# Performance work log

Measured on AMD Instinct MI355X. Metric: run time of the kernel, lower is better.

## Reference

```python
import jax, jax.numpy as jnp
import numpy as np

N_FEAT = 11   # players+ball features
HID = 48      # GAT hidden dim
HEADS = 4
GRU = 64
B = 64        # chains
T = 16        # frames per chain
NPG = 23      # nodes per frame graph (22 players + ball)
G = B * T
NTOT = G * NPG
FRAME = 2 * HID  # mean||max pool


def setup_inputs() -> dict:
    key = jax.random.key(0)
    ks = jax.random.split(key, 24)
    # block-diagonal fully-connected (with self loops) edge_index per graph
    base = np.arange(NPG)
    src = np.repeat(base, NPG)
    dst = np.tile(base, NPG)
    off = (np.arange(G) * NPG)[:, None]
    edge_index = np.stack([(src[None] + off).ravel(), (dst[None] + off).ravel()]).astype(np.int64)
    batch = np.repeat(np.arange(G), NPG).astype(np.int64)

    def p(k, shape, scale=0.1):
        return jax.random.normal(k, shape, jnp.float32) * scale

    return dict(
        x=jax.random.normal(ks[0], (NTOT, N_FEAT), jnp.float32),
        edge_index=jnp.asarray(edge_index), batch=jnp.asarray(batch),
        W1=p(ks[1], (N_FEAT, HEADS * HID)), as1=p(ks[2], (HEADS, HID)), ad1=p(ks[3], (HEADS, HID)), b1=p(ks[4], (HEADS * HID,)),
        W2=p(ks[5], (HEADS * HID, HID)), as2=p(ks[6], (1, HID)), ad2=p(ks[7], (1, HID)), b2=p(ks[8], (HID,)),
        Wih0=p(ks[9], (3 * GRU, FRAME)), Whh0=p(ks[10], (3 * GRU, GRU)), bih0=p(ks[11], (3 * GRU,)), bhh0=p(ks[12], (3 * GRU,)),
        Wih1=p(ks[13], (3 * GRU, GRU)), Whh1=p(ks[14], (3 * GRU, GRU)), bih1=p(ks[15], (3 * GRU,)), bhh1=p(ks[16], (3 * GRU,)),
        Wh1=p(ks[17], (GRU, 32)), bh1=p(ks[18], (32,)), Wh2=p(ks[19], (32, 1)), bh2=p(ks[20], (1,)),
    )


def _gat(x, src, dst, W, a_s, a_d, b, heads, concat):
    # PyG GATConv: per-head linear, edge score LeakyReLU(a_s.h_i + a_d.h_j),
    # softmax over incoming edges (by dst), weighted aggregation of h_src.
    h = (x @ W).reshape(-1, heads, HID)            # [N,H,D]
    al_s = (h * a_s).sum(-1)                       # [N,H]
    al_d = (h * a_d).sum(-1)
    e = jax.nn.leaky_relu(al_s[src] + al_d[dst], 0.2)  # [E,H]
    m = jax.ops.segment_max(e, dst, num_segments=NTOT)
    w = jnp.exp(e - m[dst])
    s = jax.ops.segment_sum(w, dst, num_segments=NTOT)
    alpha = w / (s[dst] + 1e-16)
    out = jax.ops.segment_sum(h[src] * alpha[:, :, None], dst, num_segments=NTOT)  # [N,H,D]
    if concat:
        return out.reshape(NTOT, heads * HID) + b
    return out.mean(1) + b


def _gru_layer(xs, Wih, Whh, bih, bhh):
    # torch.nn.GRU single layer, batch_first; xs: [B,T,in]
    def step(h, x_t):
        gi = x_t @ Wih.T + bih
        gh = h @ Whh.T + bhh
        ir, iz, in_ = jnp.split(gi, 3, -1)
        hr, hz, hn = jnp.split(gh, 3, -1)
        r = jax.nn.sigmoid(ir + hr)
        z = jax.nn.sigmoid(iz + hz)
        n = jnp.tanh(in_ + r * hn)
        h2 = (1 - z) * n + z * h
        return h2, h2
    h0 = jnp.zeros((xs.shape[0], GRU), xs.dtype)
    _, out = jax.lax.scan(step, h0, jnp.swapaxes(xs, 0, 1))
    return jnp.swapaxes(out, 0, 1)


def reference(x, edge_index, batch, W1, as1, ad1, b1, W2, as2, ad2, b2,
              Wih0, Whh0, bih0, bhh0, Wih1, Whh1, bih1, bhh1, Wh1, bh1, Wh2, bh2):
    src, dst = edge_index[0], edge_index[1]
    h = jax.nn.elu(_gat(x, src, dst, W1, as1, ad1, b1, HEADS, True))   # [N,192]
    h = jax.nn.elu(_gat(h, src, dst, W2, as2, ad2, b2, 1, False))      # [N,48]
    mean = jax.ops.segment_sum(h, batch, num_segments=G) / NPG
    mx = jax.ops.segment_max(h, batch, num_segments=G)
    frames = jnp.concatenate([mean, mx], -1).reshape(B, T, FRAME)      # [B,T,96]
    h1 = _gru_layer(frames, Wih0, Whh0, bih0, bhh0)
    h2 = _gru_layer(h1, Wih1, Whh1, bih1, bhh1)
    last = h2[:, -1]                                                   # [B,64]
    logits = jax.nn.relu(last @ Wh1 + bh1) @ Wh2 + bh2                 # [B,1]
    return logits[:, 0]
```

## Files before the change

### kernel.cpp

```cpp
#include <hip/hip_runtime.h>
#include <math.h>

#define NPG    23
#define HID    48
#define HEADS  4
#define C1     192
#define NFEAT  11
#define GG     1024
#define GRUH   64
#define FRAME  96
#define TT     16
#define BB     64

#define HSTR   196
#define GSTR   52

#define OFF_X    0
#define OFF_ALS  256
#define OFF_ALD  348
#define OFF_H    440
#define OFF_H1   4948
#define LDSF     9456

__device__ __forceinline__ float elu_(float v) {
    return (v > 0.f) ? v : (__expf(v) - 1.f);
}

#define PHASE_FENCE() __builtin_amdgcn_sched_barrier(0)

__global__ __launch_bounds__(256, 2) void gat_fused(
    const float* __restrict__ x,
    const float* __restrict__ W1,
    const float* __restrict__ as1,
    const float* __restrict__ ad1,
    const float* __restrict__ b1,
    const float* __restrict__ W2,
    const float* __restrict__ as2,
    const float* __restrict__ ad2,
    const float* __restrict__ b2,
    float* __restrict__ frames)
{
    __shared__ float S[LDSF];
    float* s_x    = S + OFF_X;
    float* s_als  = S + OFF_ALS;
    float* s_ald  = S + OFF_ALD;
    float* s_h    = S + OFF_H;
    float* s_h1   = S + OFF_H1;
    float* s_g    = S + OFF_H;
    float* s_h2   = S + OFF_H + NPG * GSTR;
    float* s_als2 = S + OFF_X;
    float* s_ald2 = S + OFF_X + NPG;

    const int g   = blockIdx.x;
    const int tid = threadIdx.x;

    for (int i = tid; i < NPG * NFEAT; i += 256) s_x[i] = x[g * NPG * NFEAT + i];
    if (tid < 184) s_als[tid] = 0.f;
    __syncthreads();
    PHASE_FENCE();

    if (tid < 240) {
        const int c4 = tid % 48, ng = tid / 48;
        const int hh = c4 / 12;
        float4 acc[5];
        #pragma unroll
        for (int nn = 0; nn < 5; nn++) acc[nn] = make_float4(0.f, 0.f, 0.f, 0.f);
        #pragma unroll 1
        for (int k = 0; k < NFEAT; k++) {
            const float4 w = *(const float4*)(W1 + k * C1 + 4 * c4);
            #pragma unroll
            for (int nn = 0; nn < 5; nn++) {
                int n = ng * 5 + nn; n = (n < NPG) ? n : NPG - 1;
                const float xv = s_x[n * NFEAT + k];
                acc[nn].x += xv * w.x; acc[nn].y += xv * w.y;
                acc[nn].z += xv * w.z; acc[nn].w += xv * w.w;
            }
        }
        const float4 a_s = *(const float4*)(as1 + 4 * c4);
        const float4 a_d = *(const float4*)(ad1 + 4 * c4);
        #pragma unroll
        for (int nn = 0; nn < 5; nn++) {
            const int n = ng * 5 + nn;
            if (n < NPG) {
                *(float4*)(s_h + n * HSTR + 4 * c4) = acc[nn];
                atomicAdd(&s_als[hh * NPG + n],
                          acc[nn].x * a_s.x + acc[nn].y * a_s.y + acc[nn].z * a_s.z + acc[nn].w * a_s.w);
                atomicAdd(&s_ald[hh * NPG + n],
                          acc[nn].x * a_d.x + acc[nn].y * a_d.y + acc[nn].z * a_d.z + acc[nn].w * a_d.w);
            }
        }
    }
    __syncthreads();
    PHASE_FENCE();

    if (tid < 184) {
        const int j = tid >> 3, sub = tid & 7;
        const int hh = sub >> 1, half = sub & 1;
        const float ald_j = s_ald[hh * NPG + j];
        float a[NPG];
        float m = -1e30f;
        #pragma unroll
        for (int i = 0; i < NPG; i++) {
            float e = s_als[hh * NPG + i] + ald_j;
            e = (e > 0.f) ? e : 0.2f * e;
            a[i] = e;
            m = fmaxf(m, e);
        }
        float ssum = 0.f;
        #pragma unroll
        for (int i = 0; i < NPG; i++) {
            const float w = __expf(a[i] - m);
            a[i] = w;
            ssum += w;
        }
        const float inv = 1.f / (ssum + 1e-16f);
        const int cb = hh * HID + half * 24;
        #pragma unroll 1
        for (int c4 = 0; c4 < 6; c4++) {
            float4 acc = make_float4(0.f, 0.f, 0.f, 0.f);
            #pragma unroll
            for (int i = 0; i < NPG; i++) {
                const float4 hv = *(const float4*)(s_h + i * HSTR + cb + 4 * c4);
                acc.x += a[i] * hv.x; acc.y += a[i] * hv.y;
                acc.z += a[i] * hv.z; acc.w += a[i] * hv.w;
            }
            const float4 bb = *(const float4*)(b1 + cb + 4 * c4);
            float4 v;
            v.x = elu_(acc.x * inv + bb.x);
            v.y = elu_(acc.y * inv + bb.y);
            v.z = elu_(acc.z * inv + bb.z);
            v.w = elu_(acc.w * inv + bb.w);
            *(float4*)(s_h1 + j * HSTR + cb + 4 * c4) = v;
        }
    } else if (tid < 184 + 46) {
        s_als2[tid - 184] = 0.f;
    }
    __syncthreads();
    PHASE_FENCE();

    if (tid < 192) {
        const int kc  = tid & 3;
        const int rem = tid >> 2;
        const int c4  = rem % 12, ng = rem / 12;
        float4 acc[6];
        #pragma unroll
        for (int nn = 0; nn < 6; nn++) acc[nn] = make_float4(0.f, 0.f, 0.f, 0.f);
        #pragma unroll 1
        for (int k4 = 0; k4 < 12; k4++) {
            const int kk = kc * 12 + k4;
            const float* w2p = W2 + (4 * kk) * HID + 4 * c4;
            const float4 r0 = *(const float4*)(w2p);
            const float4 r1 = *(const float4*)(w2p + HID);
            const float4 r2 = *(const float4*)(w2p + 2 * HID);
            const float4 r3 = *(const float4*)(w2p + 3 * HID);
            #pragma unroll
            for (int nn = 0; nn < 6; nn++) {
                int n = ng * 6 + nn; n = (n < NPG) ? n : NPG - 1;
                const float4 hv = *(const float4*)(s_h1 + n * HSTR + 4 * kk);
                acc[nn].x += hv.x*r0.x + hv.y*r1.x + hv.z*r2.x + hv.w*r3.x;
                acc[nn].y += hv.x*r0.y + hv.y*r1.y + hv.z*r2.y + hv.w*r3.y;
                acc[nn].z += hv.x*r0.z + hv.y*r1.z + hv.z*r2.z + hv.w*r3.z;
                acc[nn].w += hv.x*r0.w + hv.y*r1.w + hv.z*r2.w + hv.w*r3.w;
            }
        }
        #pragma unroll
        for (int nn = 0; nn < 6; nn++) {
            float4 a = acc[nn];
            a.x += __shfl_xor(a.x, 1); a.x += __shfl_xor(a.x, 2);
            a.y += __shfl_xor(a.y, 1); a.y += __shfl_xor(a.y, 2);
            a.z += __shfl_xor(a.z, 1); a.z += __shfl_xor(a.z, 2);
            a.w += __shfl_xor(a.w, 1); a.w += __shfl_xor(a.w, 2);
            acc[nn] = a;
        }
        if (kc == 0) {
            const float4 a_s = *(const float4*)(as2 + 4 * c4);
            const float4 a_d = *(const float4*)(ad2 + 4 * c4);
            #pragma unroll
            for (int nn = 0; nn < 6; nn++) {
                const int n = ng * 6 + nn;
                if (n < NPG) {
                    *(float4*)(s_g + n * GSTR + 4 * c4) = acc[nn];
                    atomicAdd(&s_als2[n],
                              acc[nn].x*a_s.x + acc[nn].y*a_s.y + acc[nn].z*a_s.z + acc[nn].w*a_s.w);
                    atomicAdd(&s_ald2[n],
                              acc[nn].x*a_d.x + acc[nn].y*a_d.y + acc[nn].z*a_d.z + acc[nn].w*a_d.w);
                }
            }
        }
    }
    __syncthreads();
    PHASE_FENCE();

    if (tid < 48) {
        const int q = tid & 3, jp = tid >> 2;
        const int j0 = 2 * jp, j1 = 2 * jp + 1;
        const bool has1 = (j1 < NPG);
        const int cb = q * 12;
        const float ald0 = s_ald2[j0];
        const float ald1 = has1 ? s_ald2[j1] : 0.f;
        float m0 = -1e30f, m1 = -1e30f;
        #pragma unroll
        for (int i = 0; i < NPG; i++) {
            const float ai = s_als2[i];
            float e0 = ai + ald0; e0 = (e0 > 0.f) ? e0 : 0.2f * e0;
            float e1 = ai + ald1; e1 = (e1 > 0.f) ? e1 : 0.2f * e1;
            m0 = fmaxf(m0, e0); m1 = fmaxf(m1, e1);
        }
        float4 acc0[3], acc1[3];
        #pragma unroll
        for (int c = 0; c < 3; c++) {
            acc0[c] = make_float4(0.f, 0.f, 0.f, 0.f);
            acc1[c] = make_float4(0.f, 0.f, 0.f, 0.f);
        }
        float ss0 = 0.f, ss1 = 0.f;
        #pragma unroll 1
        for (int i = 0; i < NPG; i++) {
            const float ai = s_als2[i];
            float e0 = ai + ald0; e0 = (e0 > 0.f) ? e0 : 0.2f * e0;
            float e1 = ai + ald1; e1 = (e1 > 0.f) ? e1 : 0.2f * e1;
            const float p0 = __expf(e0 - m0); ss0 += p0;
            const float p1 = __expf(e1 - m1); ss1 += p1;
            const float* gp = s_g + i * GSTR + cb;
            #pragma unroll
            for (int c = 0; c < 3; c++) {
                const float4 gv = *(const float4*)(gp + 4 * c);
                acc0[c].x += p0 * gv.x; acc0[c].y += p0 * gv.y;
                acc0[c].z += p0 * gv.z; acc0[c].w += p0 * gv.w;
                acc1[c].x += p1 * gv.x; acc1[c].y += p1 * gv.y;
                acc1[c].z += p1 * gv.z; acc1[c].w += p1 * gv.w;
            }
        }
        const float inv0 = 1.f / (ss0 + 1e-16f);
        const float inv1 = 1.f / (ss1 + 1e-16f);
        #pragma unroll
        for (int c = 0; c < 3; c++) {
            const float4 bb = *(const float4*)(b2 + cb + 4 * c);
            float4 v;
            v.x = elu_(acc0[c].x * inv0 + bb.x);
            v.y = elu_(acc0[c].y * inv0 + bb.y);
            v.z = elu_(acc0[c].z * inv0 + bb.z);
            v.w = elu_(acc0[c].w * inv0 + bb.w);
            *(float4*)(s_h2 + j0 * HID + cb + 4 * c) = v;
            if (has1) {
                v.x = elu_(acc1[c].x * inv1 + bb.x);
                v.y = elu_(acc1[c].y * inv1 + bb.y);
                v.z = elu_(acc1[c].z * inv1 + bb.z);
                v.w = elu_(acc1[c].w * inv1 + bb.w);
                *(float4*)(s_h2 + j1 * HID + cb + 4 * c) = v;
            }
        }
    }
    __syncthreads();
    PHASE_FENCE();

    if (tid < HID) {
        float sm = 0.f, mx = -1e30f;
        #pragma unroll
        for (int j = 0; j < NPG; j++) {
            const float v = s_h2[j * HID + tid];
            sm += v; mx = fmaxf(mx, v);
        }
        frames[g * FRAME + tid]       = sm * (1.0f / NPG);
        frames[g * FRAME + HID + tid] = mx;
    }
}

__global__ __launch_bounds__(384) void gru_head(
    const float* __restrict__ frames,
    const float* __restrict__ Wih0,
    const float* __restrict__ bih0,
    const float* __restrict__ Whh0,
    const float* __restrict__ bhh0,
    const float* __restrict__ Wih1,
    const float* __restrict__ bih1,
    const float* __restrict__ Whh1,
    const float* __restrict__ bhh1,
    const float* __restrict__ Wh1,
    const float* __restrict__ bh1,
    const float* __restrict__ Wh2,
    const float* __restrict__ bh2,
    float* __restrict__ out)
{
    __shared__ float s_f[TT * FRAME];
    __shared__ float s_gi0[TT * C1];
    __shared__ float s_h0[GRUH], s_h1[GRUH];
    __shared__ float s_gh0[C1], s_gi1[C1], s_gh1[C1];
    __shared__ float s_t1[32];

    const int b = blockIdx.x, tid = threadIdx.x;

    {
        const float4* src = (const float4*)(frames + b * TT * FRAME);
        ((float4*)s_f)[tid] = src[tid];
    }
    if (tid < GRUH) { s_h0[tid] = 0.f; s_h1[tid] = 0.f; }
    __syncthreads();

    {
        const int c = tid % C1, tp = tid / C1;
        float accg[8];
        const float b0 = bih0[c];
        #pragma unroll
        for (int tt = 0; tt < 8; tt++) accg[tt] = b0;
        const float4* wr = (const float4*)(Wih0 + c * FRAME);
        const float4* f4 = (const float4*)s_f;
        #pragma unroll 4
        for (int k4 = 0; k4 < FRAME / 4; k4++) {
            const float4 w = wr[k4];
            #pragma unroll
            for (int tt = 0; tt < 8; tt++) {
                const float4 f = f4[(tt * 2 + tp) * (FRAME / 4) + k4];
                accg[tt] += w.x * f.x + w.y * f.y + w.z * f.z + w.w * f.w;
            }
        }
        #pragma unroll
        for (int tt = 0; tt < 8; tt++) s_gi0[(tt * 2 + tp) * C1 + c] = accg[tt];
    }

    const int row = tid >> 1, kh = tid & 1;
    float w0[32], w1[32], w2[32];
    {
        const float4* p0 = (const float4*)(Whh0 + row * 64 + kh * 32);
        const float4* p1 = (const float4*)(Wih1 + row * 64 + kh * 32);
        const float4* p2 = (const float4*)(Whh1 + row * 64 + kh * 32);
        #pragma unroll
        for (int k4 = 0; k4 < 8; k4++) {
            const float4 v0 = p0[k4];
            w0[4*k4] = v0.x; w0[4*k4+1] = v0.y; w0[4*k4+2] = v0.z; w0[4*k4+3] = v0.w;
            const float4 v1 = p1[k4];
            w1[4*k4] = v1.x; w1[4*k4+1] = v1.y; w1[4*k4+2] = v1.z; w1[4*k4+3] = v1.w;
            const float4 v2 = p2[k4];
            w2[4*k4] = v2.x; w2[4*k4+1] = v2.y; w2[4*k4+2] = v2.z; w2[4*k4+3] = v2.w;
        }
    }
    const float bh0r = kh ? 0.f : bhh0[row];
    const float bi1r = kh ? 0.f : bih1[row];
    const float bh1r = kh ? 0.f : bhh1[row];
    __syncthreads();

    for (int it = 0; it <= TT; it++) {
        {
            float s0 = bh0r, s1 = bi1r, s2 = bh1r;
            const float4* h0v = (const float4*)(s_h0 + kh * 32);
            const float4* h1v = (const float4*)(s_h1 + kh * 32);
            #pragma unroll
            for (int k4 = 0; k4 < 8; k4++) {
                const float4 a = h0v[k4];
                const float4 c = h1v[k4];
                s0 += w0[4*k4]*a.x + w0[4*k4+1]*a.y + w0[4*k4+2]*a.z + w0[4*k4+3]*a.w;
                s1 += w1[4*k4]*a.x + w1[4*k4+1]*a.y + w1[4*k4+2]*a.z + w1[4*k4+3]*a.w;
                s2 += w2[4*k4]*c.x + w2[4*k4+1]*c.y + w2[4*k4+2]*c.z + w2[4*k4+3]*c.w;
            }
            s0 += __shfl_xor(s0, 1, 64);
            s1 += __shfl_xor(s1, 1, 64);
            s2 += __shfl_xor(s2, 1, 64);
            if (kh == 0) { s_gh0[row] = s0; s_gi1[row] = s1; s_gh1[row] = s2; }
        }
        __syncthreads();
        if (tid < GRUH) {
            if (it < TT) {
                const float ir = s_gi0[it*C1 + tid];
                const float iz = s_gi0[it*C1 + 64 + tid];
                const float in_ = s_gi0[it*C1 + 128 + tid];
                const float hr = s_gh0[tid], hz = s_gh0[64 + tid], hn = s_gh0[128 + tid];
                const float r = 1.f / (1.f + __expf(-(ir + hr)));
                const float z = 1.f / (1.f + __expf(-(iz + hz)));
                const float nx = in_ + r * hn;
                const float e2 = __expf(2.f * nx);
                const float n = (e2 - 1.f) / (e2 + 1.f);
                s_h0[tid] = (1.f - z) * n + z * s_h0[tid];
            }
        } else if (tid < 2 * GRUH) {
            if (it >= 1) {
                const int c = tid - GRUH;
                const float ir = s_gi1[c], iz = s_gi1[64 + c], in_ = s_gi1[128 + c];
                const float hr = s_gh1[c], hz = s_gh1[64 + c], hn = s_gh1[128 + c];
                const float r = 1.f / (1.f + __expf(-(ir + hr)));
                const float z = 1.f / (1.f + __expf(-(iz + hz)));
                const float nx = in_ + r * hn;
                const float e2 = __expf(2.f * nx);
                const float n = (e2 - 1.f) / (e2 + 1.f);
                s_h1[c] = (1.f - z) * n + z * s_h1[c];
            }
        }
        __syncthreads();
    }

    if (tid < 32) {
        float s = bh1[tid];
        #pragma unroll
        for (int k = 0; k < GRUH; k++) s += s_h1[k] * Wh1[k * 32 + tid];
        s_t1[tid] = fmaxf(s, 0.f);
    }
    __syncthreads();
    if (tid == 0) {
        float s = bh2[0];
        #pragma unroll
        for (int k = 0; k < 32; k++) s += s_t1[k] * Wh2[k];
        out[b] = s;
    }
}

extern "C" void kernel_launch(void* const* d_in, const int* in_sizes, int n_in,
                              void* d_out, int out_size, void* d_ws, size_t ws_size,
                              hipStream_t stream) {
    const float* x    = (const float*)d_in[0];
    const float* W1   = (const float*)d_in[3];
    const float* as1  = (const float*)d_in[4];
    const float* ad1  = (const float*)d_in[5];
    const float* b1   = (const float*)d_in[6];
    const float* W2   = (const float*)d_in[7];
    const float* as2  = (const float*)d_in[8];
    const float* ad2  = (const float*)d_in[9];
    const float* b2   = (const float*)d_in[10];
    const float* Wih0 = (const float*)d_in[11];
    const float* Whh0 = (const float*)d_in[12];
    const float* bih0 = (const float*)d_in[13];
    const float* bhh0 = (const float*)d_in[14];
    const float* Wih1 = (const float*)d_in[15];
    const float* Whh1 = (const float*)d_in[16];
    const float* bih1 = (const float*)d_in[17];
    const float* bhh1 = (const float*)d_in[18];
    const float* Wh1  = (const float*)d_in[19];
    const float* bh1  = (const float*)d_in[20];
    const float* Wh2  = (const float*)d_in[21];
    const float* bh2  = (const float*)d_in[22];

    float* out    = (float*)d_out;
    float* frames = (float*)d_ws;

    hipLaunchKernelGGL(gat_fused, dim3(GG), dim3(256), 0, stream,
                       x, W1, as1, ad1, b1, W2, as2, ad2, b2, frames);
    hipLaunchKernelGGL(gru_head, dim3(BB), dim3(384), 0, stream,
                       frames, Wih0, bih0, Whh0, bhh0, Wih1, bih1, Whh1, bhh1,
                       Wh1, bh1, Wh2, bh2, out);
}
```

Measured before the change: 70.56 us.

## Widen GAT blocks to 512 threads and fuse GRU input projection into GAT kernel

Doubles the GAT kernel's block size to 512 threads and re-partitions every phase (linear, attention, second GAT, pooling) across more threads with fewer nodes per thread. It also moves the layer-0 GRU input projection (Wih0·frame + bih0) out of the serial 64-block GRU kernel into the per-graph GAT kernel, which writes gi0 directly. This is meant to shorten the latency-bound GRU kernel and raise parallelism in the GAT phases. The cost is a larger intermediate buffer (192 floats per graph instead of 96) and more Wih0 reads spread across 1024 blocks.

```diff
diff --git a/kernel.cpp b/kernel.cpp
--- a/kernel.cpp
+++ b/kernel.cpp
@@ -28,7 +28,7 @@
 
 #define PHASE_FENCE() __builtin_amdgcn_sched_barrier(0)
 
-__global__ __launch_bounds__(256, 2) void gat_fused(
+__global__ __launch_bounds__(512, 2) void gat_fused(
     const float* __restrict__ x,
     const float* __restrict__ W1,
     const float* __restrict__ as1,
@@ -38,7 +38,9 @@
     const float* __restrict__ as2,
     const float* __restrict__ ad2,
     const float* __restrict__ b2,
-    float* __restrict__ frames)
+    const float* __restrict__ Wih0,
+    const float* __restrict__ bih0,
+    float* __restrict__ gi0)
 {
     __shared__ float S[LDSF];
     float* s_x    = S + OFF_X;
@@ -50,27 +52,31 @@
     float* s_h2   = S + OFF_H + NPG * GSTR;
     float* s_als2 = S + OFF_X;
     float* s_ald2 = S + OFF_X + NPG;
+    float* s_frame= S + OFF_X;
 
     const int g   = blockIdx.x;
     const int tid = threadIdx.x;
 
-    for (int i = tid; i < NPG * NFEAT; i += 256) s_x[i] = x[g * NPG * NFEAT + i];
-    if (tid < 184) s_als[tid] = 0.f;
-    __syncthreads();
-    PHASE_FENCE();
-
-    if (tid < 240) {
+    if (tid < NPG * NFEAT) s_x[tid] = x[g * NPG * NFEAT + tid];
+    {
+        const int z = tid - 256;
+        if (z >= 0 && z < 184) s_als[z] = 0.f;
+    }
+    __syncthreads();
+    PHASE_FENCE();
+
+    if (tid < 384) {
         const int c4 = tid % 48, ng = tid / 48;
         const int hh = c4 / 12;
-        float4 acc[5];
-        #pragma unroll
-        for (int nn = 0; nn < 5; nn++) acc[nn] = make_float4(0.f, 0.f, 0.f, 0.f);
+        float4 acc[3];
+        #pragma unroll
+        for (int nn = 0; nn < 3; nn++) acc[nn] = make_float4(0.f, 0.f, 0.f, 0.f);
         #pragma unroll 1
         for (int k = 0; k < NFEAT; k++) {
             const float4 w = *(const float4*)(W1 + k * C1 + 4 * c4);
             #pragma unroll
-            for (int nn = 0; nn < 5; nn++) {
-                int n = ng * 5 + nn; n = (n < NPG) ? n : NPG - 1;
+            for (int nn = 0; nn < 3; nn++) {
+                int n = ng * 3 + nn; n = (n < NPG) ? n : NPG - 1;
                 const float xv = s_x[n * NFEAT + k];
                 acc[nn].x += xv * w.x; acc[nn].y += xv * w.y;
                 acc[nn].z += xv * w.z; acc[nn].w += xv * w.w;
@@ -79,8 +85,8 @@
         const float4 a_s = *(const float4*)(as1 + 4 * c4);
         const float4 a_d = *(const float4*)(ad1 + 4 * c4);
         #pragma unroll
-        for (int nn = 0; nn < 5; nn++) {
-            const int n = ng * 5 + nn;
+        for (int nn = 0; nn < 3; nn++) {
+            const int n = ng * 3 + nn;
             if (n < NPG) {
                 *(float4*)(s_h + n * HSTR + 4 * c4) = acc[nn];
                 atomicAdd(&s_als[hh * NPG + n],
@@ -93,58 +99,64 @@
     __syncthreads();
     PHASE_FENCE();
 
-    if (tid < 184) {
-        const int j = tid >> 3, sub = tid & 7;
-        const int hh = sub >> 1, half = sub & 1;
+    if (tid < 368) {
+        const int j = tid >> 4, sub = tid & 15;
+        const int hh = sub >> 2, q = sub & 3;
+        const int cb = hh * HID + q * 12;
+        const float* alsb = s_als + hh * NPG;
         const float ald_j = s_ald[hh * NPG + j];
-        float a[NPG];
         float m = -1e30f;
-        #pragma unroll
         for (int i = 0; i < NPG; i++) {
-            float e = s_als[hh * NPG + i] + ald_j;
+            float e = alsb[i] + ald_j;
             e = (e > 0.f) ? e : 0.2f * e;
-            a[i] = e;
             m = fmaxf(m, e);
         }
+        float4 a0 = make_float4(0.f,0.f,0.f,0.f);
+        float4 a1 = make_float4(0.f,0.f,0.f,0.f);
+        float4 a2 = make_float4(0.f,0.f,0.f,0.f);
         float ssum = 0.f;
-        #pragma unroll
+        #pragma unroll 1
         for (int i = 0; i < NPG; i++) {
-            const float w = __expf(a[i] - m);
-            a[i] = w;
-            ssum += w;
+            float e = alsb[i] + ald_j;
+            e = (e > 0.f) ? e : 0.2f * e;
+            const float p = __expf(e - m);
+            ssum += p;
+            const float* hp = s_h + i * HSTR + cb;
+            const float4 h0 = *(const float4*)(hp);
+            const float4 h1v = *(const float4*)(hp + 4);
+            const float4 h2v = *(const float4*)(hp + 8);
+            a0.x += p*h0.x;  a0.y += p*h0.y;  a0.z += p*h0.z;  a0.w += p*h0.w;
+            a1.x += p*h1v.x; a1.y += p*h1v.y; a1.z += p*h1v.z; a1.w += p*h1v.w;
+            a2.x += p*h2v.x; a2.y += p*h2v.y; a2.z += p*h2v.z; a2.w += p*h2v.w;
         }
         const float inv = 1.f / (ssum + 1e-16f);
-        const int cb = hh * HID + half * 24;
-        #pragma unroll 1
-        for (int c4 = 0; c4 < 6; c4++) {
-            float4 acc = make_float4(0.f, 0.f, 0.f, 0.f);
-            #pragma unroll
-            for (int i = 0; i < NPG; i++) {
-                const float4 hv = *(const float4*)(s_h + i * HSTR + cb + 4 * c4);
-                acc.x += a[i] * hv.x; acc.y += a[i] * hv.y;
-                acc.z += a[i] * hv.z; acc.w += a[i] * hv.w;
-            }
-            const float4 bb = *(const float4*)(b1 + cb + 4 * c4);
-            float4 v;
-            v.x = elu_(acc.x * inv + bb.x);
-            v.y = elu_(acc.y * inv + bb.y);
-            v.z = elu_(acc.z * inv + bb.z);
-            v.w = elu_(acc.w * inv + bb.w);
-            *(float4*)(s_h1 + j * HSTR + cb + 4 * c4) = v;
-        }
-    } else if (tid < 184 + 46) {
-        s_als2[tid - 184] = 0.f;
-    }
-    __syncthreads();
-    PHASE_FENCE();
-
-    if (tid < 192) {
-        const int kc  = tid & 3;
-        const int rem = tid >> 2;
-        const int c4  = rem % 12, ng = rem / 12;
-        float4 acc[6];
-        #pragma unroll
-        for (int nn = 0; nn < 6; nn++) acc[nn] = make_float4(0.f, 0.f, 0.f, 0.f);
+        const float4 b0 = *(const float4*)(b1 + cb);
+        const float4 b1v = *(const float4*)(b1 + cb + 4);
+        const float4 b2v = *(const float4*)(b1 + cb + 8);
+        float4 v;
+        v.x = elu_(a0.x*inv + b0.x);  v.y = elu_(a0.y*inv + b0.y);
+        v.z = elu_(a0.z*inv + b0.z);  v.w = elu_(a0.w*inv + b0.w);
+        *(float4*)(s_h1 + j * HSTR + cb) = v;
+        v.x = elu_(a1.x*inv + b1v.x); v.y = elu_(a1.y*inv + b1v.y);
+        v.z = elu_(a1.z*inv + b1v.z); v.w = elu_(a1.w*inv + b1v.w);
+        *(float4*)(s_h1 + j * HSTR + cb + 4) = v;
+        v.x = elu_(a2.x*inv + b2v.x); v.y = elu_(a2.y*inv + b2v.y);
+        v.z = elu_(a2.z*inv + b2v.z); v.w = elu_(a2.w*inv + b2v.w);
+        *(float4*)(s_h1 + j * HSTR + cb + 8) = v;
+    } else {
+        const int z = tid - 384;
+        if (z < 46) s_als2[z] = 0.f;
+    }
+    __syncthreads();
+    PHASE_FENCE();
+
+    if (tid < 384) {
+        const int kc = tid & 3;
+        const int c4 = (tid >> 2) % 12;
+        const int ng = tid / 48;
+        float4 acc[3];
+        #pragma unroll
+        for (int nn = 0; nn < 3; nn++) acc[nn] = make_float4(0.f, 0.f, 0.f, 0.f);
         #pragma unroll 1
         for (int k4 = 0; k4 < 12; k4++) {
             const int kk = kc * 12 + k4;
@@ -154,8 +166,8 @@
             const float4 r2 = *(const float4*)(w2p + 2 * HID);
             const float4 r3 = *(const float4*)(w2p + 3 * HID);
             #pragma unroll
-            for (int nn = 0; nn < 6; nn++) {
-                int n = ng * 6 + nn; n = (n < NPG) ? n : NPG - 1;
+            for (int nn = 0; nn < 3; nn++) {
+                int n = ng * 3 + nn; n = (n < NPG) ? n : NPG - 1;
                 const float4 hv = *(const float4*)(s_h1 + n * HSTR + 4 * kk);
                 acc[nn].x += hv.x*r0.x + hv.y*r1.x + hv.z*r2.x + hv.w*r3.x;
                 acc[nn].y += hv.x*r0.y + hv.y*r1.y + hv.z*r2.y + hv.w*r3.y;
@@ -164,7 +176,7 @@
             }
         }
         #pragma unroll
-        for (int nn = 0; nn < 6; nn++) {
+        for (int nn = 0; nn < 3; nn++) {
             float4 a = acc[nn];
             a.x += __shfl_xor(a.x, 1); a.x += __shfl_xor(a.x, 2);
             a.y += __shfl_xor(a.y, 1); a.y += __shfl_xor(a.y, 2);
@@ -176,8 +188,8 @@
             const float4 a_s = *(const float4*)(as2 + 4 * c4);
             const float4 a_d = *(const float4*)(ad2 + 4 * c4);
             #pragma unroll
-            for (int nn = 0; nn < 6; nn++) {
-                const int n = ng * 6 + nn;
+            for (int nn = 0; nn < 3; nn++) {
+                const int n = ng * 3 + nn;
                 if (n < NPG) {
                     *(float4*)(s_g + n * GSTR + 4 * c4) = acc[nn];
                     atomicAdd(&s_als2[n],
@@ -191,84 +203,75 @@
     __syncthreads();
     PHASE_FENCE();
 
-    if (tid < 48) {
-        const int q = tid & 3, jp = tid >> 2;
-        const int j0 = 2 * jp, j1 = 2 * jp + 1;
-        const bool has1 = (j1 < NPG);
-        const int cb = q * 12;
-        const float ald0 = s_ald2[j0];
-        const float ald1 = has1 ? s_ald2[j1] : 0.f;
-        float m0 = -1e30f, m1 = -1e30f;
-        #pragma unroll
+    if (tid < 276) {
+        const int j = tid / 12, c4 = tid % 12;
+        const int cb = 4 * c4;
+        const float ald_j = s_ald2[j];
+        float m = -1e30f;
         for (int i = 0; i < NPG; i++) {
-            const float ai = s_als2[i];
-            float e0 = ai + ald0; e0 = (e0 > 0.f) ? e0 : 0.2f * e0;
-            float e1 = ai + ald1; e1 = (e1 > 0.f) ? e1 : 0.2f * e1;
-            m0 = fmaxf(m0, e0); m1 = fmaxf(m1, e1);
-        }
-        float4 acc0[3], acc1[3];
-        #pragma unroll
-        for (int c = 0; c < 3; c++) {
-            acc0[c] = make_float4(0.f, 0.f, 0.f, 0.f);
-            acc1[c] = make_float4(0.f, 0.f, 0.f, 0.f);
-        }
-        float ss0 = 0.f, ss1 = 0.f;
+            float e = s_als2[i] + ald_j;
+            e = (e > 0.f) ? e : 0.2f * e;
+            m = fmaxf(m, e);
+        }
+        float4 acc = make_float4(0.f, 0.f, 0.f, 0.f);
+        float ssum = 0.f;
         #pragma unroll 1
         for (int i = 0; i < NPG; i++) {
-            const float ai = s_als2[i];
-            float e0 = ai + ald0; e0 = (e0 > 0.f) ? e0 : 0.2f * e0;
-            float e1 = ai + ald1; e1 = (e1 > 0.f) ? e1 : 0.2f * e1;
-            const float p0 = __expf(e0 - m0); ss0 += p0;
-            const float p1 = __expf(e1 - m1); ss1 += p1;
-            const float* gp = s_g + i * GSTR + cb;
-            #pragma unroll
-            for (int c = 0; c < 3; c++) {
-                const float4 gv = *(const float4*)(gp + 4 * c);
-                acc0[c].x += p0 * gv.x; acc0[c].y += p0 * gv.y;
-                acc0[c].z += p0 * gv.z; acc0[c].w += p0 * gv.w;
-                acc1[c].x += p1 * gv.x; acc1[c].y += p1 * gv.y;
-                acc1[c].z += p1 * gv.z; acc1[c].w += p1 * gv.w;
-            }
-        }
-        const float inv0 = 1.f / (ss0 + 1e-16f);
-        const float inv1 = 1.f / (ss1 + 1e-16f);
-        #pragma unroll
-        for (int c = 0; c < 3; c++) {
-            const float4 bb = *(const float4*)(b2 + cb + 4 * c);
-            float4 v;
-            v.x = elu_(acc0[c].x * inv0 + bb.x);
-            v.y = elu_(acc0[c].y * inv0 + bb.y);
-            v.z = elu_(acc0[c].z * inv0 + bb.z);
-            v.w = elu_(acc0[c].w * inv0 + bb.w);
-            *(float4*)(s_h2 + j0 * HID + cb + 4 * c) = v;
-            if (has1) {
-                v.x = elu_(acc1[c].x * inv1 + bb.x);
-                v.y = elu_(acc1[c].y * inv1 + bb.y);
-                v.z = elu_(acc1[c].z * inv1 + bb.z);
-                v.w = elu_(acc1[c].w * inv1 + bb.w);
-                *(float4*)(s_h2 + j1 * HID + cb + 4 * c) = v;
-            }
-        }
-    }
-    __syncthreads();
-    PHASE_FENCE();
-
-    if (tid < HID) {
-        float sm = 0.f, mx = -1e30f;
-        #pragma unroll
-        for (int j = 0; j < NPG; j++) {
-            const float v = s_h2[j * HID + tid];
-            sm += v; mx = fmaxf(mx, v);
-        }
-        frames[g * FRAME + tid]       = sm * (1.0f / NPG);
-        frames[g * FRAME + HID + tid] = mx;
+            float e = s_als2[i] + ald_j;
+            e = (e > 0.f) ? e : 0.2f * e;
+            const float p = __expf(e - m);
+            ssum += p;
+            const float4 gv = *(const float4*)(s_g + i * GSTR + cb);
+            acc.x += p * gv.x; acc.y += p * gv.y;
+            acc.z += p * gv.z; acc.w += p * gv.w;
+        }
+        const float inv = 1.f / (ssum + 1e-16f);
+        const float4 bb = *(const float4*)(b2 + cb);
+        float4 v;
+        v.x = elu_(acc.x * inv + bb.x);
+        v.y = elu_(acc.y * inv + bb.y);
+        v.z = elu_(acc.z * inv + bb.z);
+        v.w = elu_(acc.w * inv + bb.w);
+        *(float4*)(s_h2 + j * HID + cb) = v;
+    }
+    __syncthreads();
+    PHASE_FENCE();
+
+    if (tid < 96) {
+        const int col = tid % 48, half = tid / 48;
+        if (half == 0) {
+            float sm = 0.f;
+            #pragma unroll
+            for (int j = 0; j < NPG; j++) sm += s_h2[j * HID + col];
+            s_frame[col] = sm * (1.0f / NPG);
+        } else {
+            float mx = -1e30f;
+            #pragma unroll
+            for (int j = 0; j < NPG; j++) mx = fmaxf(mx, s_h2[j * HID + col]);
+            s_frame[HID + col] = mx;
+        }
+    }
+    __syncthreads();
+    PHASE_FENCE();
+
+    if (tid < 384) {
+        const int c = tid >> 1, kh = tid & 1;
+        const float4* wr = (const float4*)(Wih0 + c * FRAME + kh * 48);
+        const float4* fr = (const float4*)(s_frame + kh * 48);
+        float s = 0.f;
+        #pragma unroll 1
+        for (int k4 = 0; k4 < 12; k4++) {
+            const float4 w = wr[k4];
+            const float4 f = fr[k4];
+            s += w.x * f.x + w.y * f.y + w.z * f.z + w.w * f.w;
+        }
+        s += __shfl_xor(s, 1);
+        if (kh == 0) gi0[g * C1 + c] = s + bih0[c];
     }
 }
 
 __global__ __launch_bounds__(384) void gru_head(
-    const float* __restrict__ frames,
-    const float* __restrict__ Wih0,
-    const float* __restrict__ bih0,
+    const float* __restrict__ gi0g,
     const float* __restrict__ Whh0,
     const float* __restrict__ bhh0,
     const float* __restrict__ Wih1,
@@ -281,7 +284,6 @@
     const float* __restrict__ bh2,
     float* __restrict__ out)
 {
-    __shared__ float s_f[TT * FRAME];
     __shared__ float s_gi0[TT * C1];
     __shared__ float s_h0[GRUH], s_h1[GRUH];
     __shared__ float s_gh0[C1], s_gi1[C1], s_gh1[C1];
@@ -290,32 +292,12 @@
     const int b = blockIdx.x, tid = threadIdx.x;
 
     {
-        const float4* src = (const float4*)(frames + b * TT * FRAME);
-        ((float4*)s_f)[tid] = src[tid];
+        const float4* src = (const float4*)(gi0g + b * TT * C1);
+        float4* dst = (float4*)s_gi0;
+        dst[tid]       = src[tid];
+        dst[tid + 384] = src[tid + 384];
     }
     if (tid < GRUH) { s_h0[tid] = 0.f; s_h1[tid] = 0.f; }
-    __syncthreads();
-
-    {
-        const int c = tid % C1, tp = tid / C1;
-        float accg[8];
-        const float b0 = bih0[c];
-        #pragma unroll
-        for (int tt = 0; tt < 8; tt++) accg[tt] = b0;
-        const float4* wr = (const float4*)(Wih0 + c * FRAME);
-        const float4* f4 = (const float4*)s_f;
-        #pragma unroll 4
-        for (int k4 = 0; k4 < FRAME / 4; k4++) {
-            const float4 w = wr[k4];
-            #pragma unroll
-            for (int tt = 0; tt < 8; tt++) {
-                const float4 f = f4[(tt * 2 + tp) * (FRAME / 4) + k4];
-                accg[tt] += w.x * f.x + w.y * f.y + w.z * f.z + w.w * f.w;
-            }
-        }
-        #pragma unroll
-        for (int tt = 0; tt < 8; tt++) s_gi0[(tt * 2 + tp) * C1 + c] = accg[tt];
-    }
 
     const int row = tid >> 1, kh = tid & 1;
     float w0[32], w1[32], w2[32];
@@ -426,12 +408,12 @@
     const float* Wh2  = (const float*)d_in[21];
     const float* bh2  = (const float*)d_in[22];
 
-    float* out    = (float*)d_out;
-    float* frames = (float*)d_ws;
-
-    hipLaunchKernelGGL(gat_fused, dim3(GG), dim3(256), 0, stream,
-                       x, W1, as1, ad1, b1, W2, as2, ad2, b2, frames);
+    float* out  = (float*)d_out;
+    float* gi0  = (float*)d_ws;
+
+    hipLaunchKernelGGL(gat_fused, dim3(GG), dim3(512), 0, stream,
+                       x, W1, as1, ad1, b1, W2, as2, ad2, b2, Wih0, bih0, gi0);
     hipLaunchKernelGGL(gru_head, dim3(BB), dim3(384), 0, stream,
-                       frames, Wih0, bih0, Whh0, bhh0, Wih1, bih1, Whh1, bhh1,
+                       gi0, Whh0, bhh0, Wih1, bih1, Whh1, bhh1,
                        Wh1, bh1, Wh2, bh2, out);
 }
```

New measurement: 91.39 us. +29.5%, slower.
